# Kernel tuning notes

Measured on AMD Instinct MI355X. Metric: run time of the kernel, lower is better.

Reference implementation:

```python
import jax, jax.numpy as jnp
import numpy as np

B, N, C = 4, 4096, 16
HID, HEADS, OUT = 64, 4, 64
NEG = -1e16

def setup_inputs() -> dict:
    key = jax.random.key(0)
    ks = jax.random.split(key, 7)
    x = jax.random.normal(ks[0], (B, N, C), dtype=jnp.float32)
    # sparse-ish binary adjacency with self-loops, stored dense as in the torch module
    graph = (jax.random.randint(ks[1], (N, N), 0, 2)).astype(jnp.float32)
    graph = jnp.maximum(graph, jnp.eye(N, dtype=jnp.float32))
    # per-head Linear weights (bias=False) and the per-layer bias parameter b
    Ws = jax.random.normal(ks[2], (HEADS, C, HID), dtype=jnp.float32)   # W.weight.T per head
    bs = jax.random.normal(ks[3], (HEADS, HID), dtype=jnp.float32)
    W_out = jax.random.normal(ks[4], (HEADS * HID, OUT), dtype=jnp.float32)
    b_out = jax.random.normal(ks[5], (OUT,), dtype=jnp.float32)
    return {"x": x, "graph": graph, "Ws": Ws, "bs": bs, "W_out": W_out, "b_out": b_out}

def _gat_layer(x, graph, W, b):
    # x: [B,N,Cin], W: [Cin,D], b: [D]
    h = jnp.einsum('bnc,cd->bnd', x, W)                      # [B,N,D]
    s = jnp.einsum('bnd,bmd->bnm', h, h) * graph[None]       # [B,N,N]
    s = jnp.where(s == 0.0, NEG, s)                          # masked_fill(eq 0, -1e16)
    attn = jax.nn.softmax(s, axis=2)
    return jnp.einsum('bnm,bmd->bnd', attn, h) + b

def _leaky_relu(x):
    return jnp.where(x >= 0, x, 0.2 * x)

def reference(x, graph, Ws, bs, W_out, b_out):
    # multi-head layers, concatenated on feature dim (head-major)
    heads = jax.vmap(lambda W, b: _gat_layer(x, graph, W, b))(Ws, bs)  # [H,B,N,D]
    cat = jnp.transpose(heads, (1, 2, 0, 3)).reshape(B, N, HEADS * HID)
    cat = _leaky_relu(cat)
    out = _gat_layer(cat, graph, W_out, b_out)
    return _leaky_relu(out)
```

## Files before the change

### kernel.cpp

```cpp
#include <hip/hip_runtime.h>

typedef unsigned short u16;
typedef unsigned int u32;
typedef unsigned long long u64;
typedef __attribute__((ext_vector_type(8))) short bf16x8;
typedef __attribute__((ext_vector_type(4))) float f32x4;
typedef __attribute__((ext_vector_type(16))) float f32x16;

#define NEGF  -1.0e38f
#define MINIT -1.0e30f
#define LOG2E 1.4426950408889634f

__device__ __forceinline__ u16 f2bf(float x) {
  union { float f; u32 u; } v; v.f = x;
  u32 r = v.u + 0x7fffu + ((v.u >> 16) & 1u);
  return (u16)(r >> 16);
}
__device__ __forceinline__ float bf2f(u16 b) {
  union { u32 u; float f; } v; v.u = ((u32)b) << 16;
  return v.f;
}
__device__ __forceinline__ float bcast(u32 u) {
  union { u32 u; float f; } v; v.u = u; return v.f;
}
__device__ __forceinline__ u32 cvtpk(float a, float b) {
  u32 r;
  asm("v_cvt_pk_bf16_f32 %0, %1, %2" : "=v"(r) : "v"(a), "v"(b));
  return r;
}
__device__ __forceinline__ float fmax3(float a, float b, float c) {
  return fmaxf(fmaxf(a, b), c);
}
__device__ __forceinline__ float leaky(float x) { return x >= 0.f ? x : 0.2f * x; }

__device__ __forceinline__ void gload16(const void* g, void* l) {
  __builtin_amdgcn_global_load_lds(
      (const __attribute__((address_space(1))) u32*)(unsigned long long)g,
      (__attribute__((address_space(3))) u32*)(u32)(unsigned long long)l,
      16, 0, 0);
}

#define GRP   1040
#define TILE  8320
#define KA_OFF 0
#define KB_OFF 8320
#define KC_OFF 16640
#define V_OFF  24960
#define SMEM_BYTES 58240

__global__ __launch_bounds__(256) void pack_kernel(const float* __restrict__ graph,
                                                   u64* __restrict__ bits) {
  const int n = blockIdx.x;
  const int w = threadIdx.x >> 6, lane = threadIdx.x & 63;
  const float* gr = graph + (size_t)n * 4096;
  for (int j = 0; j < 16; ++j) {
    const int wd = j * 4 + w;
    u64 m = __ballot(gr[wd * 64 + lane] != 0.0f);
    if (lane == 0) bits[(size_t)n * 64 + wd] = m;
  }
}

__global__ __launch_bounds__(256) void h1_kernel(const float* __restrict__ x,
                                                 const float* __restrict__ Ws,
                                                 u16* __restrict__ h1a, u16* __restrict__ h1b,
                                                 u16* __restrict__ h1c) {
  const int blk = blockIdx.x;
  const int h = threadIdx.x >> 6, d = threadIdx.x & 63;
  const float* xr = x + (size_t)blk * 16;
  const float* Wp = Ws + h * (16 * 64) + d;
  float acc = 0.f;
  #pragma unroll
  for (int c = 0; c < 16; ++c) acc += xr[c] * Wp[c * 64];
  const int b = blk >> 12, n = blk & 4095;
  const size_t o = ((size_t)(b * 4 + h) * 4096 + n) * 64 + d;
  u16 a = f2bf(acc);
  float r1 = acc - bf2f(a);
  u16 bq = f2bf(r1);
  float r2 = r1 - bf2f(bq);
  h1a[o] = a; h1b[o] = bq; h1c[o] = f2bf(r2);
}

__global__ __launch_bounds__(256) void transpose_kernel(const u16* __restrict__ src,
                                                        u16* __restrict__ dst) {
  const int p = blockIdx.y, n0 = blockIdx.x * 64;
  const u16* s = src + (size_t)p * 4096 * 64;
  u16* d = dst + (size_t)p * 4096 * 64;
  __shared__ u16 tile[64][66];
  const int col = threadIdx.x & 63, r4 = threadIdx.x >> 6;
  #pragma unroll
  for (int i = 0; i < 16; ++i) {
    const int r = i * 4 + r4;
    tile[r][col] = s[(size_t)(n0 + r) * 64 + col];
  }
  __syncthreads();
  const int cs = (col & 51) | ((col & 4) << 1) | ((col & 8) >> 1);
  #pragma unroll
  for (int i = 0; i < 16; ++i) {
    const int r = i * 4 + r4;
    d[(size_t)r * 4096 + n0 + cs] = tile[col][r];
  }
}

__global__ __launch_bounds__(256) void h2_kernel(const float* __restrict__ cat,
                                                 const float* __restrict__ Wout,
                                                 u16* __restrict__ h2a, u16* __restrict__ h2b,
                                                 u16* __restrict__ h2c) {
  const int row = blockIdx.x * 4 + (threadIdx.x >> 6);
  const int d = threadIdx.x & 63;
  const float* cr = cat + (size_t)row * 256;
  float acc = 0.f;
  for (int c4 = 0; c4 < 64; ++c4) {
    const float4 cv = *(const float4*)(cr + c4 * 4);
    acc += cv.x * Wout[(c4 * 4 + 0) * 64 + d];
    acc += cv.y * Wout[(c4 * 4 + 1) * 64 + d];
    acc += cv.z * Wout[(c4 * 4 + 2) * 64 + d];
    acc += cv.w * Wout[(c4 * 4 + 3) * 64 + d];
  }
  const size_t o = (size_t)row * 64 + d;
  u16 a = f2bf(acc);
  float r1 = acc - bf2f(a);
  u16 bq = f2bf(r1);
  float r2 = r1 - bf2f(bq);
  h2a[o] = a; h2b[o] = bq; h2c[o] = f2bf(r2);
}

template <int LAYER>
__global__ __launch_bounds__(256) void attn_kernel(
    const u16* __restrict__ Ha, const u16* __restrict__ Hb, const u16* __restrict__ Hc,
    const u16* __restrict__ HaT, const u16* __restrict__ HbT,
    const u64* __restrict__ bits, const float* __restrict__ bias,
    float* __restrict__ outp, float* __restrict__ pm, float* __restrict__ pl) {
  constexpr int NCH = (LAYER == 1) ? 64 : 16;
  const int orig = blockIdx.x + 32 * blockIdx.y;
  const int sid = (orig & 7) * 64 + (orig >> 3);
  const int bx = sid & 31;
  const int py = sid >> 5;
  const int pass = (LAYER == 1) ? py : (py & 3);
  const int chg0 = (LAYER == 1) ? 0 : ((py >> 2) * 16);

  const int t = threadIdx.x;
  const int wq = t >> 6;
  const int lane = t & 63;
  const int c = lane & 31;
  const int g1 = lane >> 5;
  const int qbase = bx * 128 + wq * 32;
  const int q = qbase + c;
  const size_t poffb = (size_t)pass * (4096 * 64) * 2;

  __shared__ f32x4 smem_v[SMEM_BYTES / 16];
  char* smem = (char*)smem_v;

  const int srow = lane >> 3;
  const int scol = ((lane & 7) ^ srow) << 4;
  const char* gKa = (const char*)Ha + poffb;
  const char* gKb = (const char*)Hb + poffb;
  const char* gKc = (const char*)Hc + poffb;
  const char* gVa = (const char*)HaT + poffb;
  const char* gVb = (const char*)HbT + poffb;

  auto stageK = [&](int chg) {
    const size_t cb = (size_t)chg * 8192;
    #pragma unroll
    for (int ii = 0; ii < 2; ++ii) {
      const int g = wq * 2 + ii;
      const size_t so = cb + (size_t)(g * 8 + srow) * 128 + scol;
      const int dofs = g * GRP;
      gload16(gKa + so, smem + KA_OFF + dofs);
      gload16(gKb + so, smem + KB_OFF + dofs);
      gload16(gKc + so, smem + KC_OFF + dofs);
    }
  };
  auto stageV = [&](int chg, int buf) {
    const char* gsrc = (wq >> 1) ? gVb : gVa;
    char* dbase = smem + V_OFF + buf * 16640 + (wq >> 1) * TILE;
    const size_t cb = (size_t)chg * 128;
    #pragma unroll
    for (int ii = 0; ii < 4; ++ii) {
      const int g = (wq & 1) * 4 + ii;
      const size_t so = cb + (size_t)(g * 8 + srow) * 8192 + scol;
      gload16(gsrc + so, dbase + g * GRP);
    }
  };

  bf16x8 qf[3][4];
  {
    const char* qra = (const char*)Ha + poffb + (size_t)q * 128 + 16 * g1;
    const char* qrb = (const char*)Hb + poffb + (size_t)q * 128 + 16 * g1;
    const char* qrc = (const char*)Hc + poffb + (size_t)q * 128 + 16 * g1;
    #pragma unroll
    for (int kk = 0; kk < 4; ++kk) {
      qf[0][kk] = *(const bf16x8*)(qra + kk * 32);
      qf[1][kk] = *(const bf16x8*)(qrb + kk * 32);
      qf[2][kk] = *(const bf16x8*)(qrc + kk * 32);
    }
  }

  const u64* bqp = bits + (size_t)q * 64;

  const int swz = (c & 7) << 4;
  int iK[4];
  #pragma unroll
  for (int kk = 0; kk < 4; ++kk)
    iK[kk] = c * 128 + ((c >> 3) << 4) + ((32 * kk + 16 * g1) ^ swz);

  f32x16 Of0, Of1;
  #pragma unroll
  for (int r = 0; r < 16; ++r) { Of0[r] = 0.f; Of1[r] = 0.f; }
  float mrow = MINIT, lrow = 0.f;

  stageK(chg0);
  stageV(chg0, 0);
  u64 mcur = bqp[chg0];
  asm volatile("s_waitcnt vmcnt(0)" ::: "memory");
  __syncthreads();

  #pragma unroll 1
  for (int ch = 0; ch < NCH; ++ch) {
    const int chg = chg0 + ch;
    __builtin_amdgcn_sched_barrier(0);
    f32x16 s0, s1;
    #pragma unroll
    for (int r = 0; r < 16; ++r) { s0[r] = 0.f; s1[r] = 0.f; }
    __builtin_amdgcn_s_setprio(1);
    #pragma unroll
    for (int kk = 0; kk < 4; ++kk) {
      #pragma unroll
      for (int mt = 0; mt < 2; ++mt) {
        const char* kp = smem + mt * (4 * GRP) + iK[kk];
        const bf16x8 ka = *(const bf16x8*)(kp + KA_OFF);
        const bf16x8 kb = *(const bf16x8*)(kp + KB_OFF);
        const bf16x8 kc = *(const bf16x8*)(kp + KC_OFF);
        f32x16& sa = mt ? s1 : s0;
        sa = __builtin_amdgcn_mfma_f32_32x32x16_bf16(ka, qf[2][kk], sa, 0, 0, 0);
        sa = __builtin_amdgcn_mfma_f32_32x32x16_bf16(kb, qf[1][kk], sa, 0, 0, 0);
        sa = __builtin_amdgcn_mfma_f32_32x32x16_bf16(kc, qf[0][kk], sa, 0, 0, 0);
        sa = __builtin_amdgcn_mfma_f32_32x32x16_bf16(ka, qf[1][kk], sa, 0, 0, 0);
        sa = __builtin_amdgcn_mfma_f32_32x32x16_bf16(kb, qf[0][kk], sa, 0, 0, 0);
        sa = __builtin_amdgcn_mfma_f32_32x32x16_bf16(ka, qf[0][kk], sa, 0, 0, 0);
      }
    }
    __builtin_amdgcn_s_setprio(0);
    __builtin_amdgcn_sched_barrier(0);
    __builtin_amdgcn_s_barrier();
    __builtin_amdgcn_sched_barrier(0);
    if (ch + 1 < NCH) {
      stageK(chg + 1);
      stageV(chg + 1, (ch + 1) & 1);
    }
    __builtin_amdgcn_sched_barrier(0);

    const u32 a0 = (u32)(mcur >> (4 * g1));
    const u32 a1 = (u32)(mcur >> (32 + 4 * g1));
    #pragma unroll
    for (int r = 0; r < 16; ++r) {
      const int off = (r & 3) + 8 * (r >> 2);
      s0[r] = ((a0 >> off) & 1u) ? s0[r] : NEGF;
      s1[r] = ((a1 >> off) & 1u) ? s1[r] : NEGF;
    }
    float t0 = fmax3(s0[0], s0[1], s0[2]);
    float t1 = fmax3(s0[3], s0[4], s0[5]);
    float t2 = fmax3(s0[6], s0[7], s0[8]);
    float t3 = fmax3(s0[9], s0[10], s0[11]);
    float t4 = fmax3(s0[12], s0[13], s0[14]);
    float t5 = fmax3(s0[15], s1[0], s1[1]);
    float t6 = fmax3(s1[2], s1[3], s1[4]);
    float t7 = fmax3(s1[5], s1[6], s1[7]);
    float t8 = fmax3(s1[8], s1[9], s1[10]);
    float t9 = fmax3(s1[11], s1[12], s1[13]);
    float ta = fmaxf(s1[14], s1[15]);
    float u0 = fmax3(t0, t1, t2);
    float u1 = fmax3(t3, t4, t5);
    float u2 = fmax3(t6, t7, t8);
    float u3 = fmax3(t9, ta, u0);
    float mm = fmax3(u1, u2, u3);
    mm = fmaxf(mm, __shfl_xor(mm, 32));
    if (!__all(mm <= mrow + 8.f)) {
      const float mn = fmaxf(mrow, mm);
      const float scl = exp2f((mrow - mn) * LOG2E);
      #pragma unroll
      for (int r = 0; r < 16; ++r) { Of0[r] *= scl; Of1[r] *= scl; }
      lrow *= scl;
      mrow = mn;
    }
    #pragma unroll
    for (int r = 0; r < 16; ++r) {
      s0[r] = exp2f((s0[r] - mrow) * LOG2E);
      s1[r] = exp2f((s1[r] - mrow) * LOG2E);
    }
    {
      float r4[4];
      #pragma unroll
      for (int j = 0; j < 4; ++j)
        r4[j] = ((s0[4*j] + s0[4*j+1]) + (s0[4*j+2] + s0[4*j+3]))
              + ((s1[4*j] + s1[4*j+1]) + (s1[4*j+2] + s1[4*j+3]));
      float rs = (r4[0] + r4[1]) + (r4[2] + r4[3]);
      rs += __shfl_xor(rs, 32);
      lrow += rs;
    }

    bf16x8 pa[4], pb[4];
    #pragma unroll
    for (int kk = 0; kk < 4; ++kk) {
      const f32x16& sm = (kk >> 1) ? s1 : s0;
      const int rb = 8 * (kk & 1);
      union { u32 w[4]; bf16x8 v; } ua, ub;
      #pragma unroll
      for (int j = 0; j < 4; ++j) {
        const float p0 = sm[rb + 2*j], p1 = sm[rb + 2*j + 1];
        const u32 h = cvtpk(p0, p1);
        ua.w[j] = h;
        const float h0f = bcast(h << 16);
        const float h1f = bcast(h & 0xffff0000u);
        ub.w[j] = cvtpk(p0 - h0f, p1 - h1f);
      }
      pa[kk] = ua.v; pb[kk] = ub.v;
    }

    const char* vbase = smem + V_OFF + (ch & 1) * 16640;
    __builtin_amdgcn_s_setprio(1);
    #pragma unroll
    for (int dt = 0; dt < 2; ++dt) {
      f32x16& o = dt ? Of1 : Of0;
      #pragma unroll
      for (int kk = 0; kk < 4; ++kk) {
        const char* vp = vbase + dt * (4 * GRP) + iK[kk];
        const bf16x8 va = *(const bf16x8*)(vp);
        const bf16x8 vb = *(const bf16x8*)(vp + TILE);
        o = __builtin_amdgcn_mfma_f32_32x32x16_bf16(vb, pa[kk], o, 0, 0, 0);
        o = __builtin_amdgcn_mfma_f32_32x32x16_bf16(va, pb[kk], o, 0, 0, 0);
        o = __builtin_amdgcn_mfma_f32_32x32x16_bf16(va, pa[kk], o, 0, 0, 0);
      }
    }
    __builtin_amdgcn_s_setprio(0);

    u64 mnxt = 0;
    if (ch + 1 < NCH) mnxt = bqp[chg + 1];
    __builtin_amdgcn_sched_barrier(0);
    if (ch + 1 < NCH) {
      asm volatile("s_waitcnt vmcnt(1)" ::: "memory");
    } else {
      asm volatile("s_waitcnt vmcnt(0)" ::: "memory");
    }
    __builtin_amdgcn_sched_barrier(0);
    __builtin_amdgcn_s_barrier();
    mcur = mnxt;
  }

  char* reg = smem + wq * 8704;
  const float inv = (LAYER == 1) ? (1.0f / lrow) : 1.0f;
  #pragma unroll
  for (int dt = 0; dt < 2; ++dt) {
    const f32x16& o = dt ? Of1 : Of0;
    #pragma unroll
    for (int i = 0; i < 4; ++i) {
      f32x4 v;
      v[0] = o[4*i+0] * inv; v[1] = o[4*i+1] * inv;
      v[2] = o[4*i+2] * inv; v[3] = o[4*i+3] * inv;
      *(f32x4*)(reg + c * 272 + (32 * dt + 8 * i + 4 * g1) * 4) = v;
    }
  }
  if (LAYER == 2 && lane < 32) {
    pm[(size_t)py * 4096 + q] = mrow;
    pl[(size_t)py * 4096 + q] = lrow;
  }
  __syncthreads();
  const int d0 = (lane & 15) * 4;
  const float* bp = (LAYER == 1) ? (bias + (pass & 3) * 64) : bias;
  #pragma unroll
  for (int qq = 0; qq < 8; ++qq) {
    const int ql = qq * 4 + (lane >> 4);
    f32x4 v = *(const f32x4*)(reg + ql * 272 + (lane & 15) * 16);
    const int qg = qbase + ql;
    if (LAYER == 1) {
      v[0] = leaky(v[0] + bp[d0 + 0]);
      v[1] = leaky(v[1] + bp[d0 + 1]);
      v[2] = leaky(v[2] + bp[d0 + 2]);
      v[3] = leaky(v[3] + bp[d0 + 3]);
      *(f32x4*)&outp[((size_t)((pass >> 2) * 4096 + qg)) * 256 + (pass & 3) * 64 + d0] = v;
    } else {
      *(f32x4*)&outp[((size_t)py * 4096 + qg) * 64 + d0] = v;
    }
  }
}

__global__ __launch_bounds__(256) void merge_kernel(
    const float* __restrict__ pO, const float* __restrict__ pm, const float* __restrict__ pl,
    const float* __restrict__ bo, float* __restrict__ dout) {
  const int t = threadIdx.x;
  const int d = t & 63;
  const int q = blockIdx.x * 4 + (t >> 6);
  const int pass = blockIdx.y;
  float m[4], l[4], o[4];
  #pragma unroll
  for (int s = 0; s < 4; ++s) {
    const size_t idx = (size_t)(s * 4 + pass) * 4096 + q;
    m[s] = pm[idx]; l[s] = pl[idx];
    o[s] = pO[idx * 64 + d];
  }
  const float M = fmaxf(fmaxf(m[0], m[1]), fmaxf(m[2], m[3]));
  float num = 0.f, den = 0.f;
  #pragma unroll
  for (int s = 0; s < 4; ++s) {
    const float w = exp2f((m[s] - M) * LOG2E);
    num += w * o[s]; den += w * l[s];
  }
  const float r = num / den + bo[d];
  dout[((size_t)pass * 4096 + q) * 64 + d] = leaky(r);
}

extern "C" void kernel_launch(void* const* d_in, const int* in_sizes, int n_in,
                              void* d_out, int out_size, void* d_ws, size_t ws_size,
                              hipStream_t stream) {
  const float* x     = (const float*)d_in[0];
  const float* graph = (const float*)d_in[1];
  const float* Ws    = (const float*)d_in[2];
  const float* bs    = (const float*)d_in[3];
  const float* W_out = (const float*)d_in[4];
  const float* b_out = (const float*)d_in[5];
  char* ws = (char*)d_ws;
  const size_t MiB = 1048576;

  u64* bits   = (u64*)(ws + 0 * MiB);
  u16* h1a    = (u16*)(ws + 2 * MiB);
  u16* h1b    = (u16*)(ws + 10 * MiB);
  u16* h1c    = (u16*)(ws + 18 * MiB);
  u16* h1aT   = (u16*)(ws + 26 * MiB);
  u16* h1bT   = (u16*)(ws + 34 * MiB);
  float* catb = (float*)(ws + 42 * MiB);
  u16* h2a    = (u16*)(ws + 58 * MiB);
  u16* h2b    = (u16*)(ws + 60 * MiB);
  u16* h2c    = (u16*)(ws + 62 * MiB);
  u16* h2aT   = (u16*)(ws + 64 * MiB);
  u16* h2bT   = (u16*)(ws + 66 * MiB);
  float* pO   = (float*)(ws + 2 * MiB);
  float* pmb  = (float*)(ws + 18 * MiB);
  float* plb  = (float*)(ws + 18 * MiB + 262144);

  pack_kernel<<<4096, 256, 0, stream>>>(graph, bits);
  h1_kernel<<<16384, 256, 0, stream>>>(x, Ws, h1a, h1b, h1c);
  transpose_kernel<<<dim3(64, 16), 256, 0, stream>>>(h1a, h1aT);
  transpose_kernel<<<dim3(64, 16), 256, 0, stream>>>(h1b, h1bT);
  attn_kernel<1><<<dim3(32, 16), 256, 0, stream>>>(h1a, h1b, h1c, h1aT, h1bT,
                                                   bits, bs, catb, nullptr, nullptr);
  h2_kernel<<<4096, 256, 0, stream>>>(catb, W_out, h2a, h2b, h2c);
  transpose_kernel<<<dim3(64, 4), 256, 0, stream>>>(h2a, h2aT);
  transpose_kernel<<<dim3(64, 4), 256, 0, stream>>>(h2b, h2bT);
  attn_kernel<2><<<dim3(32, 16), 256, 0, stream>>>(h2a, h2b, h2c, h2aT, h2bT,
                                                   bits, b_out, pO, pmb, plb);
  merge_kernel<<<dim3(1024, 4), 256, 0, stream>>>(pO, pmb, plb, b_out, (float*)d_out);
}
```

Baseline: 461.4 us.

## Interleave MFMA chains, use raw v_exp_f32, transpose adjacency bitmask layout

Reorders the QK and PV MFMA sequences so the two independent accumulator chains (s0/s1, Of0/Of1) alternate, which hides MFMA dependency latency. The first MFMA now takes a zero constant instead of an explicitly zeroed accumulator. exp2f is replaced by the raw v_exp_f32 instruction, and layer 1 folds the subtract-and-scale into an FMA. The packed adjacency bitmask is stored chunk-major so that lanes loading neighboring query rows hit contiguous addresses. The raw exp skips exp2f's denormal and range handling, which could change numerics slightly.

```diff
diff --git a/kernel.cpp b/kernel.cpp
--- a/kernel.cpp
+++ b/kernel.cpp
@@ -26,6 +26,11 @@
 __device__ __forceinline__ u32 cvtpk(float a, float b) {
   u32 r;
   asm("v_cvt_pk_bf16_f32 %0, %1, %2" : "=v"(r) : "v"(a), "v"(b));
+  return r;
+}
+__device__ __forceinline__ float vexp2(float x) {
+  float r;
+  asm("v_exp_f32 %0, %1" : "=v"(r) : "v"(x));
   return r;
 }
 __device__ __forceinline__ float fmax3(float a, float b, float c) {
@@ -56,7 +61,7 @@
   for (int j = 0; j < 16; ++j) {
     const int wd = j * 4 + w;
     u64 m = __ballot(gr[wd * 64 + lane] != 0.0f);
-    if (lane == 0) bits[(size_t)n * 64 + wd] = m;
+    if (lane == 0) bits[(size_t)wd * 4096 + n] = m;
   }
 }
 
@@ -195,7 +200,7 @@
     }
   }
 
-  const u64* bqp = bits + (size_t)q * 64;
+  const u64* bqp = bits + q;
 
   const int swz = (c & 7) << 4;
   int iK[4];
@@ -203,6 +208,7 @@
   for (int kk = 0; kk < 4; ++kk)
     iK[kk] = c * 128 + ((c >> 3) << 4) + ((32 * kk + 16 * g1) ^ swz);
 
+  const f32x16 z16 = {};
   f32x16 Of0, Of1;
   #pragma unroll
   for (int r = 0; r < 16; ++r) { Of0[r] = 0.f; Of1[r] = 0.f; }
@@ -210,7 +216,7 @@
 
   stageK(chg0);
   stageV(chg0, 0);
-  u64 mcur = bqp[chg0];
+  u64 mcur = bqp[(size_t)chg0 * 4096];
   asm volatile("s_waitcnt vmcnt(0)" ::: "memory");
   __syncthreads();
 
@@ -219,25 +225,29 @@
     const int chg = chg0 + ch;
     __builtin_amdgcn_sched_barrier(0);
     f32x16 s0, s1;
-    #pragma unroll
-    for (int r = 0; r < 16; ++r) { s0[r] = 0.f; s1[r] = 0.f; }
     __builtin_amdgcn_s_setprio(1);
     #pragma unroll
     for (int kk = 0; kk < 4; ++kk) {
-      #pragma unroll
-      for (int mt = 0; mt < 2; ++mt) {
-        const char* kp = smem + mt * (4 * GRP) + iK[kk];
-        const bf16x8 ka = *(const bf16x8*)(kp + KA_OFF);
-        const bf16x8 kb = *(const bf16x8*)(kp + KB_OFF);
-        const bf16x8 kc = *(const bf16x8*)(kp + KC_OFF);
-        f32x16& sa = mt ? s1 : s0;
-        sa = __builtin_amdgcn_mfma_f32_32x32x16_bf16(ka, qf[2][kk], sa, 0, 0, 0);
-        sa = __builtin_amdgcn_mfma_f32_32x32x16_bf16(kb, qf[1][kk], sa, 0, 0, 0);
-        sa = __builtin_amdgcn_mfma_f32_32x32x16_bf16(kc, qf[0][kk], sa, 0, 0, 0);
-        sa = __builtin_amdgcn_mfma_f32_32x32x16_bf16(ka, qf[1][kk], sa, 0, 0, 0);
-        sa = __builtin_amdgcn_mfma_f32_32x32x16_bf16(kb, qf[0][kk], sa, 0, 0, 0);
-        sa = __builtin_amdgcn_mfma_f32_32x32x16_bf16(ka, qf[0][kk], sa, 0, 0, 0);
-      }
+      const char* kp0 = smem + iK[kk];
+      const char* kp1 = smem + 4 * GRP + iK[kk];
+      const bf16x8 ka0 = *(const bf16x8*)(kp0 + KA_OFF);
+      const bf16x8 kb0 = *(const bf16x8*)(kp0 + KB_OFF);
+      const bf16x8 kc0 = *(const bf16x8*)(kp0 + KC_OFF);
+      const bf16x8 ka1 = *(const bf16x8*)(kp1 + KA_OFF);
+      const bf16x8 kb1 = *(const bf16x8*)(kp1 + KB_OFF);
+      const bf16x8 kc1 = *(const bf16x8*)(kp1 + KC_OFF);
+      s0 = __builtin_amdgcn_mfma_f32_32x32x16_bf16(ka0, qf[2][kk], kk ? s0 : z16, 0, 0, 0);
+      s1 = __builtin_amdgcn_mfma_f32_32x32x16_bf16(ka1, qf[2][kk], kk ? s1 : z16, 0, 0, 0);
+      s0 = __builtin_amdgcn_mfma_f32_32x32x16_bf16(kb0, qf[1][kk], s0, 0, 0, 0);
+      s1 = __builtin_amdgcn_mfma_f32_32x32x16_bf16(kb1, qf[1][kk], s1, 0, 0, 0);
+      s0 = __builtin_amdgcn_mfma_f32_32x32x16_bf16(kc0, qf[0][kk], s0, 0, 0, 0);
+      s1 = __builtin_amdgcn_mfma_f32_32x32x16_bf16(kc1, qf[0][kk], s1, 0, 0, 0);
+      s0 = __builtin_amdgcn_mfma_f32_32x32x16_bf16(ka0, qf[1][kk], s0, 0, 0, 0);
+      s1 = __builtin_amdgcn_mfma_f32_32x32x16_bf16(ka1, qf[1][kk], s1, 0, 0, 0);
+      s0 = __builtin_amdgcn_mfma_f32_32x32x16_bf16(kb0, qf[0][kk], s0, 0, 0, 0);
+      s1 = __builtin_amdgcn_mfma_f32_32x32x16_bf16(kb1, qf[0][kk], s1, 0, 0, 0);
+      s0 = __builtin_amdgcn_mfma_f32_32x32x16_bf16(ka0, qf[0][kk], s0, 0, 0, 0);
+      s1 = __builtin_amdgcn_mfma_f32_32x32x16_bf16(ka1, qf[0][kk], s1, 0, 0, 0);
     }
     __builtin_amdgcn_s_setprio(0);
     __builtin_amdgcn_sched_barrier(0);
@@ -276,16 +286,25 @@
     mm = fmaxf(mm, __shfl_xor(mm, 32));
     if (!__all(mm <= mrow + 8.f)) {
       const float mn = fmaxf(mrow, mm);
-      const float scl = exp2f((mrow - mn) * LOG2E);
+      const float scl = vexp2((mrow - mn) * LOG2E);
       #pragma unroll
       for (int r = 0; r < 16; ++r) { Of0[r] *= scl; Of1[r] *= scl; }
       lrow *= scl;
       mrow = mn;
     }
-    #pragma unroll
-    for (int r = 0; r < 16; ++r) {
-      s0[r] = exp2f((s0[r] - mrow) * LOG2E);
-      s1[r] = exp2f((s1[r] - mrow) * LOG2E);
+    if (LAYER == 1) {
+      const float mL = mrow * LOG2E;
+      #pragma unroll
+      for (int r = 0; r < 16; ++r) {
+        s0[r] = vexp2(__builtin_fmaf(s0[r], LOG2E, -mL));
+        s1[r] = vexp2(__builtin_fmaf(s1[r], LOG2E, -mL));
+      }
+    } else {
+      #pragma unroll
+      for (int r = 0; r < 16; ++r) {
+        s0[r] = vexp2((s0[r] - mrow) * LOG2E);
+        s1[r] = vexp2((s1[r] - mrow) * LOG2E);
+      }
     }
     {
       float r4[4];
@@ -319,22 +338,24 @@
     const char* vbase = smem + V_OFF + (ch & 1) * 16640;
     __builtin_amdgcn_s_setprio(1);
     #pragma unroll
-    for (int dt = 0; dt < 2; ++dt) {
-      f32x16& o = dt ? Of1 : Of0;
-      #pragma unroll
-      for (int kk = 0; kk < 4; ++kk) {
-        const char* vp = vbase + dt * (4 * GRP) + iK[kk];
-        const bf16x8 va = *(const bf16x8*)(vp);
-        const bf16x8 vb = *(const bf16x8*)(vp + TILE);
-        o = __builtin_amdgcn_mfma_f32_32x32x16_bf16(vb, pa[kk], o, 0, 0, 0);
-        o = __builtin_amdgcn_mfma_f32_32x32x16_bf16(va, pb[kk], o, 0, 0, 0);
-        o = __builtin_amdgcn_mfma_f32_32x32x16_bf16(va, pa[kk], o, 0, 0, 0);
-      }
+    for (int kk = 0; kk < 4; ++kk) {
+      const char* vp0 = vbase + iK[kk];
+      const char* vp1 = vbase + 4 * GRP + iK[kk];
+      const bf16x8 va0 = *(const bf16x8*)(vp0);
+      const bf16x8 vb0 = *(const bf16x8*)(vp0 + TILE);
+      const bf16x8 va1 = *(const bf16x8*)(vp1);
+      const bf16x8 vb1 = *(const bf16x8*)(vp1 + TILE);
+      Of0 = __builtin_amdgcn_mfma_f32_32x32x16_bf16(vb0, pa[kk], Of0, 0, 0, 0);
+      Of1 = __builtin_amdgcn_mfma_f32_32x32x16_bf16(vb1, pa[kk], Of1, 0, 0, 0);
+      Of0 = __builtin_amdgcn_mfma_f32_32x32x16_bf16(va0, pb[kk], Of0, 0, 0, 0);
+      Of1 = __builtin_amdgcn_mfma_f32_32x32x16_bf16(va1, pb[kk], Of1, 0, 0, 0);
+      Of0 = __builtin_amdgcn_mfma_f32_32x32x16_bf16(va0, pa[kk], Of0, 0, 0, 0);
+      Of1 = __builtin_amdgcn_mfma_f32_32x32x16_bf16(va1, pa[kk], Of1, 0, 0, 0);
     }
     __builtin_amdgcn_s_setprio(0);
 
     u64 mnxt = 0;
-    if (ch + 1 < NCH) mnxt = bqp[chg + 1];
+    if (ch + 1 < NCH) mnxt = bqp[(size_t)(chg + 1) * 4096];
     __builtin_amdgcn_sched_barrier(0);
     if (ch + 1 < NCH) {
       asm volatile("s_waitcnt vmcnt(1)" ::: "memory");
```

After: 445.0 us. 3.6% less time.
